# Kernel optimization log

Hardware: AMD Instinct MI355X
Metric: run time of the kernel (lower is better)

The kernel has to match this reference:

```python
import jax, jax.numpy as jnp
import numpy as np

N_NODES = 100_000
N_EDGES = 1_600_000
NUM_GRAPHS = 512
D1, D2, D3, D5, NUM_CLASSES = 3, 50, 15, 10, 6
BN_EPS = 1e-5


def setup_inputs() -> dict:
    key = jax.random.key(0)
    ks = jax.random.split(key, 16)

    def w(k, shape):
        fan_in = shape[0]
        return jax.random.normal(k, shape, jnp.float32) / np.sqrt(fan_in).astype(np.float32)

    return {
        "x": jax.random.normal(ks[0], (N_NODES, D1), jnp.float32),
        "edge_attr": jax.random.normal(ks[1], (N_EDGES, D1), jnp.float32),
        # edge MLP: Lin(9,50) -> ReLU -> Lin(50,15)
        "edge_w1": w(ks[2], (3 * D1, D2)), "edge_b1": jnp.zeros((D2,), jnp.float32),
        "edge_w2": w(ks[3], (D2, D3)), "edge_b2": jnp.zeros((D3,), jnp.float32),
        # node MLP: Lin(18,50) -> ReLU -> Lin(50,15)
        "node_w1": w(ks[4], (D1 + D3, D2)), "node_b1": jnp.zeros((D2,), jnp.float32),
        "node_w2": w(ks[5], (D2, D3)), "node_b2": jnp.zeros((D3,), jnp.float32),
        # readout head
        "fc1_w": w(ks[6], (D3, D5)), "fc1_b": jnp.zeros((D5,), jnp.float32),
        "bn_gamma": jnp.ones((D5,), jnp.float32), "bn_beta": jnp.zeros((D5,), jnp.float32),
        "fc2_w": w(ks[7], (D5, NUM_CLASSES)), "fc2_b": jnp.zeros((NUM_CLASSES,), jnp.float32),
        # graph structure
        "edge_index": jax.random.randint(ks[8], (2, N_EDGES), 0, N_NODES, jnp.int32),
        "batch": jnp.sort(jax.random.randint(ks[9], (N_NODES,), 0, NUM_GRAPHS, jnp.int32)),
    }


def _segment_mean(vals, idx, num_segments):
    s = jax.ops.segment_sum(vals, idx, num_segments=num_segments)
    c = jax.ops.segment_sum(jnp.ones((vals.shape[0], 1), vals.dtype), idx,
                            num_segments=num_segments)
    return s / jnp.maximum(c, 1.0)


def reference(x, edge_attr,
              edge_w1, edge_b1, edge_w2, edge_b2,
              node_w1, node_b1, node_w2, node_b2,
              fc1_w, fc1_b, bn_gamma, bn_beta, fc2_w, fc2_b,
              edge_index, batch):
    row, col = edge_index[0], edge_index[1]
    # edge model: cat([x[row], x[col], edge_attr]) -> MLP  -> [E, D3]
    e_in = jnp.concatenate([x[row], x[col], edge_attr], axis=1)
    edge_attr2 = jax.nn.relu(e_in @ edge_w1 + edge_b1) @ edge_w2 + edge_b2
    # node model: cat([x[col], edge_attr2]) -> MLP -> scatter_mean over row
    n_in = jnp.concatenate([x[col], edge_attr2], axis=1)  # [E, D1+D3]
    msg = jax.nn.relu(n_in @ node_w1 + node_b1) @ node_w2 + node_b2  # [E, D3]
    x2 = _segment_mean(msg, row, x.shape[0])  # [N, D3]
    # global mean pool per graph -> [G, D3]
    u = _segment_mean(x2, batch, NUM_GRAPHS)
    # head: fc1 -> BatchNorm1d (batch stats) -> relu -> fc2 -> log_softmax
    h = u @ fc1_w + fc1_b
    mu = h.mean(axis=0)
    var = h.var(axis=0)  # biased, matches BN training normalization
    h = bn_gamma * (h - mu) * jax.lax.rsqrt(var + BN_EPS) + bn_beta
    h = jax.nn.relu(h)
    logits = h @ fc2_w + fc2_b
    return jax.nn.log_softmax(logits, axis=1)
```

## Files before the change

### kernel.cpp

```cpp
#include <hip/hip_runtime.h>
#include <hip/hip_bf16.h>
#include <math.h>

#define N_NODES    100000
#define N_EDGES    1600000
#define NUM_GRAPHS 512
#define D2 50
#define D3 15
#define D5 10
#define NCLS 6
#define BN_EPS 1e-5f

#define NBLK1 ((N_NODES + 1023) / 1024)

#define W_EW1T 0
#define W_EW2T 2560
#define W_NW1T 3712
#define W_NW2T 6272
#define W_TOTAL 7680

#define EDGE_BLOCKS 2500
#define EDGE_WAVES  (EDGE_BLOCKS * 4)
#define TILES32     (N_EDGES / 32)
#define EDGE_ITERS  (TILES32 / EDGE_WAVES)

typedef __attribute__((ext_vector_type(8))) short short8;
typedef __attribute__((ext_vector_type(4))) float float4_;
union BU { unsigned u[4]; short8 s; };
union FU { unsigned u; float f; };

__device__ __forceinline__ unsigned short f2bf(float f) {
    __hip_bfloat16 h = __float2bfloat16(f);
    union { __hip_bfloat16 h; unsigned short u; } c; c.h = h; return c.u;
}
__device__ __forceinline__ float bf2f(unsigned short u) {
    union { __hip_bfloat16 h; unsigned short u; } c; c.u = u;
    return __bfloat162float(c.h);
}
__device__ __forceinline__ unsigned int pkbf(float a, float b) {
    return (unsigned int)f2bf(a) | ((unsigned int)f2bf(b) << 16);
}
__device__ __forceinline__ unsigned bp(int s4, unsigned v) {
    return (unsigned)__builtin_amdgcn_ds_bpermute(s4, (int)v);
}
__device__ __forceinline__ float lo16(unsigned u) { FU c; c.u = u << 16; return c.f; }
__device__ __forceinline__ float hi16(unsigned u) { FU c; c.u = u & 0xFFFF0000u; return c.f; }

__global__ __launch_bounds__(256) void prep_kernel(
    const float* __restrict__ ew1, const float* __restrict__ eb1,
    const float* __restrict__ ew2, const float* __restrict__ eb2,
    const float* __restrict__ nw1, const float* __restrict__ nb1,
    const float* __restrict__ nw2, const float* __restrict__ nb2,
    unsigned short* __restrict__ wh, unsigned short* __restrict__ wl,
    const float* __restrict__ x, ushort4* __restrict__ x4b,
    const int* __restrict__ edge_index, int* __restrict__ counts)
{
    int gtid = blockIdx.x * 256 + threadIdx.x;
    int gsz = gridDim.x * 256;

    for (int i = gtid; i < W_TOTAL; i += gsz) {
        float v = 0.0f;
        if (i < W_EW2T) {
            int m = i / 40, k = i % 40;
            if (m < 50) {
                if (k < 3)                 v = ew1[k * 50 + m];
                else if (k == 3)           v = eb1[m];
                else if (k >= 4 && k < 7)  v = ew1[(k - 1) * 50 + m];
                else if (k >= 8 && k < 11) v = ew1[(k - 2) * 50 + m];
            }
        } else if (i < W_NW1T) {
            int j = i - W_EW2T; int m = j / 72, k = j % 72;
            if (m < 15) { if (k < 50) v = ew2[k * 15 + m]; else if (k == 50) v = eb2[m]; }
        } else if (i < W_NW2T) {
            int j = i - W_NW1T; int m = j / 40, k = j % 40;
            if (m < 50) {
                if (k < 15)                  v = nw1[(3 + k) * 50 + m];
                else if (k >= 16 && k < 19)  v = nw1[(k - 16) * 50 + m];
                else if (k == 19)            v = nb1[m];
            }
        } else if (i < 7424) {
            int j = i - W_NW2T; int m = j / 72, k = j % 72;
            if (m < 15) { if (k < 50) v = nw2[k * 15 + m]; else if (k == 50) v = nb2[m]; }
        }
        unsigned short h = f2bf(v);
        unsigned short l = f2bf(v - bf2f(h));
        wh[i] = h; wl[i] = l;
    }

    for (int n = gtid; n < N_NODES; n += gsz) {
        ushort4 v;
        v.x = f2bf(x[n * 3 + 0]); v.y = f2bf(x[n * 3 + 1]);
        v.z = f2bf(x[n * 3 + 2]); v.w = 0;
        x4b[n] = v;
    }

    for (int e = gtid; e < N_EDGES; e += gsz)
        atomicAdd(&counts[edge_index[e]], 1);
}

__global__ __launch_bounds__(1024) void scan1_kernel(
    const int* __restrict__ counts, int* __restrict__ scanned, int* __restrict__ bsums)
{
    __shared__ int wsum[16], wofs[16];
    int i = blockIdx.x * 1024 + threadIdx.x;
    int lane = threadIdx.x & 63, wid = threadIdx.x >> 6;
    int v = (i < N_NODES) ? counts[i] : 0;
    int sc = v;
    #pragma unroll
    for (int off = 1; off < 64; off <<= 1) {
        int t = __shfl_up(sc, off);
        if (lane >= off) sc += t;
    }
    if (lane == 63) wsum[wid] = sc;
    __syncthreads();
    if (wid == 0) {
        int s = (lane < 16) ? wsum[lane] : 0;
        #pragma unroll
        for (int off = 1; off < 16; off <<= 1) {
            int t = __shfl_up(s, off);
            if (lane >= off) s += t;
        }
        if (lane < 16) wofs[lane] = s - wsum[lane];
    }
    __syncthreads();
    int incl = sc + wofs[wid];
    if (i < N_NODES) scanned[i] = incl - v;
    if (threadIdx.x == 1023) bsums[blockIdx.x] = incl;
}

__global__ __launch_bounds__(128) void scan2_kernel(
    const int* __restrict__ bsums, int* __restrict__ bofs)
{
    __shared__ int tmp[128];
    int v = (threadIdx.x < NBLK1) ? bsums[threadIdx.x] : 0;
    tmp[threadIdx.x] = v;
    __syncthreads();
    #pragma unroll
    for (int off = 1; off < 128; off <<= 1) {
        int t = (threadIdx.x >= off) ? tmp[threadIdx.x - off] : 0;
        __syncthreads();
        tmp[threadIdx.x] += t;
        __syncthreads();
    }
    if (threadIdx.x < NBLK1) bofs[threadIdx.x] = tmp[threadIdx.x] - v;
}

__global__ __launch_bounds__(256) void scan3_kernel(
    const int* __restrict__ scanned, const int* __restrict__ bofs,
    int* __restrict__ cursor)
{
    int n = blockIdx.x * 256 + threadIdx.x;
    if (n >= N_NODES) return;
    cursor[n] = scanned[n] + bofs[n >> 10];
}

struct EIn { unsigned w0, w1, w2, w3, h0, h1; int pos; };

__device__ __forceinline__ EIn load_in(int ebase, int n, int quad,
    const int* __restrict__ edge_index, const ushort4* __restrict__ x4b,
    const float* __restrict__ edge_attr, int* __restrict__ cursor)
{
    EIn r; r.w0 = r.w1 = r.w2 = r.w3 = 0; r.h0 = r.h1 = 0; r.pos = 0;
    int e = ebase + n;
    if (quad == 0) {
        int row = edge_index[e];
        int col = edge_index[N_EDGES + e];
        ushort4 xr = x4b[row];
        ushort4 xc = x4b[col];
        r.w0 = (unsigned)xr.x | ((unsigned)xr.y << 16);
        r.w1 = (unsigned)xr.z | (0x3F80u << 16);
        r.w2 = (unsigned)xc.x | ((unsigned)xc.y << 16);
        r.w3 = (unsigned)xc.z;
        r.pos = atomicAdd(&cursor[row], 1);
    } else if (quad == 1) {
        r.w0 = pkbf(edge_attr[e * 3 + 0], edge_attr[e * 3 + 1]);
        r.w1 = (unsigned)f2bf(edge_attr[e * 3 + 2]);
    } else if (quad == 2) {
        int col = edge_index[N_EDGES + e];
        ushort4 xc = x4b[col];
        r.h0 = (unsigned)xc.x | ((unsigned)xc.y << 16);
        r.h1 = (unsigned)xc.z | (0x3F80u << 16);
    }
    return r;
}

__device__ __forceinline__ void perm64(const unsigned U[4][2], int s0, int s1, bool hi,
                                       short8& Bc0, short8& Bc1)
{
    BU b0, b1;
    {
        unsigned a0 = bp(s0, U[0][0]), a1 = bp(s0, U[1][0]);
        unsigned a2 = bp(s0, U[0][1]), a3 = bp(s0, U[1][1]);
        unsigned a4 = bp(s1, U[0][0]), a5 = bp(s1, U[1][0]);
        unsigned a6 = bp(s1, U[0][1]), a7 = bp(s1, U[1][1]);
        b0.u[0] = hi ? a1 : a0;
        b0.u[1] = hi ? a3 : a2;
        b0.u[2] = hi ? a5 : a4;
        b0.u[3] = hi ? a7 : a6;
    }
    {
        unsigned a0 = bp(s0, U[2][0]), a1 = bp(s0, U[3][0]);
        unsigned a2 = bp(s0, U[2][1]), a3 = bp(s0, U[3][1]);
        unsigned a4 = bp(s1, U[2][0]), a5 = bp(s1, U[3][0]);
        unsigned a6 = bp(s1, U[2][1]), a7 = bp(s1, U[3][1]);
        b1.u[0] = hi ? a1 : a0;
        b1.u[1] = hi ? a3 : a2;
        b1.u[2] = hi ? a5 : a4;
        b1.u[3] = hi ? a7 : a6;
    }
    Bc0 = b0.s; Bc1 = b1.s;
}

__device__ __forceinline__ short8 perm16(const unsigned U2[2], int s0, int s1,
                                         int quad, unsigned h0, unsigned h1)
{
    BU d;
    d.u[0] = bp(s0, U2[0]);
    d.u[1] = bp(s0, U2[1]);
    d.u[2] = bp(s1, U2[0]);
    d.u[3] = bp(s1, U2[1]);
    if (quad == 2) { d.u[0] = h0; d.u[1] = h1; d.u[2] = 0; d.u[3] = 0; }
    else if (quad == 3) { d.u[0] = 0; d.u[1] = 0; d.u[2] = 0; d.u[3] = 0; }
    return d.s;
}

__global__ __launch_bounds__(256) void edge_mfma_kernel(
    const unsigned short* __restrict__ wh_g, const unsigned short* __restrict__ wl_g,
    const ushort4* __restrict__ x4b, const float* __restrict__ edge_attr,
    const int* __restrict__ edge_index,
    int* __restrict__ cursor, unsigned short* __restrict__ msgb)
{
    int tid = threadIdx.x, wave = tid >> 6, lane = tid & 63;
    int n = lane & 15, quad = lane >> 4;

    short8 A1h[4], A1l[4], A3h[4], A3l[4];
    #pragma unroll
    for (int t4 = 0; t4 < 4; t4++) {
        int o1 = W_EW1T + (t4 * 16 + n) * 40 + quad * 8;
        A1h[t4] = *(const short8*)(wh_g + o1);
        A1l[t4] = *(const short8*)(wl_g + o1);
        int o3 = W_NW1T + (t4 * 16 + n) * 40 + quad * 8;
        A3h[t4] = *(const short8*)(wh_g + o3);
        A3l[t4] = *(const short8*)(wl_g + o3);
    }
    short8 A2h[2], A2l[2], A4h[2], A4l[2];
    #pragma unroll
    for (int kc = 0; kc < 2; kc++) {
        int o2 = W_EW2T + n * 72 + kc * 32 + quad * 8;
        A2h[kc] = *(const short8*)(wh_g + o2);
        A2l[kc] = *(const short8*)(wl_g + o2);
        int o4 = W_NW2T + n * 72 + kc * 32 + quad * 8;
        A4h[kc] = *(const short8*)(wh_g + o4);
        A4l[kc] = *(const short8*)(wl_g + o4);
    }

    int s0 = ((quad & 1) * 32 + n) * 4;
    int s1 = s0 + 64;
    bool hi = (quad & 2) != 0;

    int t = blockIdx.x * 4 + wave;
    EIn cur0 = load_in(t * 32,      n, quad, edge_index, x4b, edge_attr, cursor);
    EIn cur1 = load_in(t * 32 + 16, n, quad, edge_index, x4b, edge_attr, cursor);

    for (int it = 0; it < EDGE_ITERS; it++) {
        int p0 = __shfl(cur0.pos, n);
        int p1 = __shfl(cur1.pos, n);

        int tn = t + EDGE_WAVES;
        EIn nx0, nx1;
        nx0.w0 = nx0.w1 = nx0.w2 = nx0.w3 = nx0.h0 = nx0.h1 = 0; nx0.pos = 0;
        nx1 = nx0;
        if (it + 1 < EDGE_ITERS) {
            nx0 = load_in(tn * 32,      n, quad, edge_index, x4b, edge_attr, cursor);
            nx1 = load_in(tn * 32 + 16, n, quad, edge_index, x4b, edge_attr, cursor);
        }

        BU t0, t1;
        t0.u[0] = cur0.w0; t0.u[1] = cur0.w1; t0.u[2] = cur0.w2; t0.u[3] = cur0.w3;
        t1.u[0] = cur1.w0; t1.u[1] = cur1.w1; t1.u[2] = cur1.w2; t1.u[3] = cur1.w3;
        short8 B1a = t0.s, B1b = t1.s;

        unsigned U1a[4][2], U1b[4][2];
        #pragma unroll
        for (int t4 = 0; t4 < 4; t4++) {
            float4_ za = {0.f, 0.f, 0.f, 0.f}, zb = {0.f, 0.f, 0.f, 0.f};
            za = __builtin_amdgcn_mfma_f32_16x16x32_bf16(A1l[t4], B1a, za, 0, 0, 0);
            zb = __builtin_amdgcn_mfma_f32_16x16x32_bf16(A1l[t4], B1b, zb, 0, 0, 0);
            za = __builtin_amdgcn_mfma_f32_16x16x32_bf16(A1h[t4], B1a, za, 0, 0, 0);
            zb = __builtin_amdgcn_mfma_f32_16x16x32_bf16(A1h[t4], B1b, zb, 0, 0, 0);
            U1a[t4][0] = pkbf(fmaxf(za[0], 0.f), fmaxf(za[1], 0.f));
            U1a[t4][1] = pkbf(fmaxf(za[2], 0.f), fmaxf(za[3], 0.f));
            U1b[t4][0] = pkbf(fmaxf(zb[0], 0.f), fmaxf(zb[1], 0.f));
            U1b[t4][1] = pkbf(fmaxf(zb[2], 0.f), fmaxf(zb[3], 0.f));
        }

        short8 B2a0, B2a1, B2b0, B2b1;
        perm64(U1a, s0, s1, hi, B2a0, B2a1);
        perm64(U1b, s0, s1, hi, B2b0, B2b1);
        if (quad == 2) {
            BU fa, fb; fa.s = B2a1; fb.s = B2b1;
            fa.u[1] = (fa.u[1] & 0xFFFF0000u) | 0x3F80u;
            fb.u[1] = (fb.u[1] & 0xFFFF0000u) | 0x3F80u;
            B2a1 = fa.s; B2b1 = fb.s;
        }

        float4_ a2al = {0.f, 0.f, 0.f, 0.f}, a2ah = {0.f, 0.f, 0.f, 0.f};
        float4_ a2bl = {0.f, 0.f, 0.f, 0.f}, a2bh = {0.f, 0.f, 0.f, 0.f};
        a2al = __builtin_amdgcn_mfma_f32_16x16x32_bf16(A2l[0], B2a0, a2al, 0, 0, 0);
        a2bl = __builtin_amdgcn_mfma_f32_16x16x32_bf16(A2l[0], B2b0, a2bl, 0, 0, 0);
        a2ah = __builtin_amdgcn_mfma_f32_16x16x32_bf16(A2h[0], B2a0, a2ah, 0, 0, 0);
        a2bh = __builtin_amdgcn_mfma_f32_16x16x32_bf16(A2h[0], B2b0, a2bh, 0, 0, 0);
        a2al = __builtin_amdgcn_mfma_f32_16x16x32_bf16(A2l[1], B2a1, a2al, 0, 0, 0);
        a2bl = __builtin_amdgcn_mfma_f32_16x16x32_bf16(A2l[1], B2b1, a2bl, 0, 0, 0);
        a2ah = __builtin_amdgcn_mfma_f32_16x16x32_bf16(A2h[1], B2a1, a2ah, 0, 0, 0);
        a2bh = __builtin_amdgcn_mfma_f32_16x16x32_bf16(A2h[1], B2b1, a2bh, 0, 0, 0);

        unsigned U2a[2] = { pkbf(a2al[0] + a2ah[0], a2al[1] + a2ah[1]),
                            pkbf(a2al[2] + a2ah[2], a2al[3] + a2ah[3]) };
        unsigned U2b[2] = { pkbf(a2bl[0] + a2bh[0], a2bl[1] + a2bh[1]),
                            pkbf(a2bl[2] + a2bh[2], a2bl[3] + a2bh[3]) };

        short8 B3a = perm16(U2a, s0, s1, quad, cur0.h0, cur0.h1);
        short8 B3b = perm16(U2b, s0, s1, quad, cur1.h0, cur1.h1);

        unsigned U3a[4][2], U3b[4][2];
        #pragma unroll
        for (int t4 = 0; t4 < 4; t4++) {
            float4_ za = {0.f, 0.f, 0.f, 0.f}, zb = {0.f, 0.f, 0.f, 0.f};
            za = __builtin_amdgcn_mfma_f32_16x16x32_bf16(A3l[t4], B3a, za, 0, 0, 0);
            zb = __builtin_amdgcn_mfma_f32_16x16x32_bf16(A3l[t4], B3b, zb, 0, 0, 0);
            za = __builtin_amdgcn_mfma_f32_16x16x32_bf16(A3h[t4], B3a, za, 0, 0, 0);
            zb = __builtin_amdgcn_mfma_f32_16x16x32_bf16(A3h[t4], B3b, zb, 0, 0, 0);
            U3a[t4][0] = pkbf(fmaxf(za[0], 0.f), fmaxf(za[1], 0.f));
            U3a[t4][1] = pkbf(fmaxf(za[2], 0.f), fmaxf(za[3], 0.f));
            U3b[t4][0] = pkbf(fmaxf(zb[0], 0.f), fmaxf(zb[1], 0.f));
            U3b[t4][1] = pkbf(fmaxf(zb[2], 0.f), fmaxf(zb[3], 0.f));
        }

        short8 B4a0, B4a1, B4b0, B4b1;
        perm64(U3a, s0, s1, hi, B4a0, B4a1);
        perm64(U3b, s0, s1, hi, B4b0, B4b1);
        if (quad == 2) {
            BU fa, fb; fa.s = B4a1; fb.s = B4b1;
            fa.u[1] = (fa.u[1] & 0xFFFF0000u) | 0x3F80u;
            fb.u[1] = (fb.u[1] & 0xFFFF0000u) | 0x3F80u;
            B4a1 = fa.s; B4b1 = fb.s;
        }

        float4_ mal = {0.f, 0.f, 0.f, 0.f}, mah = {0.f, 0.f, 0.f, 0.f};
        float4_ mbl = {0.f, 0.f, 0.f, 0.f}, mbh = {0.f, 0.f, 0.f, 0.f};
        mal = __builtin_amdgcn_mfma_f32_16x16x32_bf16(A4l[0], B4a0, mal, 0, 0, 0);
        mbl = __builtin_amdgcn_mfma_f32_16x16x32_bf16(A4l[0], B4b0, mbl, 0, 0, 0);
        mah = __builtin_amdgcn_mfma_f32_16x16x32_bf16(A4h[0], B4a0, mah, 0, 0, 0);
        mbh = __builtin_amdgcn_mfma_f32_16x16x32_bf16(A4h[0], B4b0, mbh, 0, 0, 0);
        mal = __builtin_amdgcn_mfma_f32_16x16x32_bf16(A4l[1], B4a1, mal, 0, 0, 0);
        mbl = __builtin_amdgcn_mfma_f32_16x16x32_bf16(A4l[1], B4b1, mbl, 0, 0, 0);
        mah = __builtin_amdgcn_mfma_f32_16x16x32_bf16(A4h[1], B4a1, mah, 0, 0, 0);
        mbh = __builtin_amdgcn_mfma_f32_16x16x32_bf16(A4h[1], B4b1, mbh, 0, 0, 0);

        uint2 pa, pb;
        pa.x = pkbf(mal[0] + mah[0], mal[1] + mah[1]);
        pa.y = pkbf(mal[2] + mah[2], mal[3] + mah[3]);
        pb.x = pkbf(mbl[0] + mbh[0], mbl[1] + mbh[1]);
        pb.y = pkbf(mbl[2] + mbh[2], mbl[3] + mbh[3]);
        *(uint2*)(msgb + (size_t)p0 * 16 + quad * 4) = pa;
        *(uint2*)(msgb + (size_t)p1 * 16 + quad * 4) = pb;

        cur0 = nx0; cur1 = nx1; t = tn;
    }
}

__global__ __launch_bounds__(256) void gather_pool_kernel(
    const unsigned short* __restrict__ msgb, const int* __restrict__ scanned,
    const int* __restrict__ bofs, const int* __restrict__ counts,
    const int* __restrict__ batch, float* __restrict__ gsum)
{
    __shared__ float acc[64 * 16];
    int n0 = blockIdx.x * 256;
    int n = n0 + threadIdx.x;

    float v[16];
    #pragma unroll
    for (int k = 0; k < 16; k++) v[k] = 0.0f;
    if (n < N_NODES) {
        int start = scanned[n] + bofs[n >> 10];
        int deg = counts[n];
        for (int j = 0; j < deg; j++) {
            const uint4* mp = (const uint4*)(msgb + (size_t)(start + j) * 16);
            uint4 qa = mp[0], qb = mp[1];
            v[0]  += lo16(qa.x); v[1]  += hi16(qa.x);
            v[2]  += lo16(qa.y); v[3]  += hi16(qa.y);
            v[4]  += lo16(qa.z); v[5]  += hi16(qa.z);
            v[6]  += lo16(qa.w); v[7]  += hi16(qa.w);
            v[8]  += lo16(qb.x); v[9]  += hi16(qb.x);
            v[10] += lo16(qb.y); v[11] += hi16(qb.y);
            v[12] += lo16(qb.z); v[13] += hi16(qb.z);
            v[14] += lo16(qb.w);
        }
        float inv = 1.0f / fmaxf((float)deg, 1.0f);
        #pragma unroll
        for (int k = 0; k < 15; k++) v[k] *= inv;
        v[15] = 1.0f;
    }

    int gmin = batch[n0];
    int gmax = batch[min(n0 + 255, N_NODES - 1)];
    int range = gmax - gmin + 1;
    if (range <= 64) {
        for (int t = threadIdx.x; t < range * 16; t += 256) acc[t] = 0.0f;
        __syncthreads();
        if (n < N_NODES) {
            int g = batch[n] - gmin;
            float* dst = &acc[g * 16];
            #pragma unroll
            for (int k = 0; k < 16; k++) atomicAdd(&dst[k], v[k]);
        }
        __syncthreads();
        for (int t = threadIdx.x; t < range * 16; t += 256) {
            float w = acc[t];
            if (w != 0.0f) atomicAdd(&gsum[(size_t)gmin * 16 + t], w);
        }
    } else {
        if (n < N_NODES) {
            int g = batch[n];
            float* dst = gsum + (size_t)g * 16;
            #pragma unroll
            for (int k = 0; k < 16; k++) atomicAdd(&dst[k], v[k]);
        }
    }
}

__global__ __launch_bounds__(512) void head_kernel(
    const float* __restrict__ gsum,
    const float* __restrict__ fc1w, const float* __restrict__ fc1b,
    const float* __restrict__ gamma, const float* __restrict__ beta,
    const float* __restrict__ fc2w, const float* __restrict__ fc2b,
    float* __restrict__ out)
{
    __shared__ float ssum[D5], ssq[D5], smu[D5], sistd[D5];
    int g = threadIdx.x;
    if (g < D5) { ssum[g] = 0.0f; ssq[g] = 0.0f; }
    __syncthreads();

    const float* src = gsum + (size_t)g * 16;
    float inv = 1.0f / fmaxf(src[15], 1.0f);
    float u[D3];
    #pragma unroll
    for (int k = 0; k < D3; k++) u[k] = src[k] * inv;

    float h[D5];
    #pragma unroll
    for (int c = 0; c < D5; c++) h[c] = fc1b[c];
    #pragma unroll
    for (int k = 0; k < D3; k++) {
        float v = u[k];
        #pragma unroll
        for (int c = 0; c < D5; c++) h[c] = fmaf(v, fc1w[k * D5 + c], h[c]);
    }

    int lane = threadIdx.x & 63;
    #pragma unroll
    for (int c = 0; c < D5; c++) {
        float v = h[c];
        float v2 = v * v;
        #pragma unroll
        for (int off = 32; off >= 1; off >>= 1) {
            v  += __shfl_xor(v,  off);
            v2 += __shfl_xor(v2, off);
        }
        if (lane == 0) { atomicAdd(&ssum[c], v); atomicAdd(&ssq[c], v2); }
    }
    __syncthreads();
    if (g < D5) {
        float mu = ssum[g] * (1.0f / NUM_GRAPHS);
        float var = ssq[g] * (1.0f / NUM_GRAPHS) - mu * mu;
        smu[g] = mu;
        sistd[g] = rsqrtf(var + BN_EPS);
    }
    __syncthreads();

    float hn[D5];
    #pragma unroll
    for (int c = 0; c < D5; c++) {
        float v = gamma[c] * (h[c] - smu[c]) * sistd[c] + beta[c];
        hn[c] = fmaxf(v, 0.0f);
    }

    float lg[NCLS];
    #pragma unroll
    for (int j = 0; j < NCLS; j++) lg[j] = fc2b[j];
    #pragma unroll
    for (int c = 0; c < D5; c++) {
        float v = hn[c];
        #pragma unroll
        for (int j = 0; j < NCLS; j++) lg[j] = fmaf(v, fc2w[c * NCLS + j], lg[j]);
    }

    float m = lg[0];
    #pragma unroll
    for (int j = 1; j < NCLS; j++) m = fmaxf(m, lg[j]);
    float se = 0.0f;
    #pragma unroll
    for (int j = 0; j < NCLS; j++) se += expf(lg[j] - m);
    float lse = logf(se);
    #pragma unroll
    for (int j = 0; j < NCLS; j++) out[g * NCLS + j] = lg[j] - m - lse;
}

extern "C" void kernel_launch(void* const* d_in, const int* in_sizes, int n_in,
                              void* d_out, int out_size, void* d_ws, size_t ws_size,
                              hipStream_t stream) {
    const float* x         = (const float*)d_in[0];
    const float* edge_attr = (const float*)d_in[1];
    const float* ew1  = (const float*)d_in[2];
    const float* eb1  = (const float*)d_in[3];
    const float* ew2  = (const float*)d_in[4];
    const float* eb2  = (const float*)d_in[5];
    const float* nw1  = (const float*)d_in[6];
    const float* nb1  = (const float*)d_in[7];
    const float* nw2  = (const float*)d_in[8];
    const float* nb2  = (const float*)d_in[9];
    const float* fc1w = (const float*)d_in[10];
    const float* fc1b = (const float*)d_in[11];
    const float* gamma= (const float*)d_in[12];
    const float* beta = (const float*)d_in[13];
    const float* fc2w = (const float*)d_in[14];
    const float* fc2b = (const float*)d_in[15];
    const int* edge_index = (const int*)d_in[16];
    const int* batch      = (const int*)d_in[17];

    char* p = (char*)d_ws;
    unsigned short* msgb = (unsigned short*)p; p += (size_t)N_EDGES * 16 * sizeof(unsigned short);
    int* counts  = (int*)p;            p += (size_t)N_NODES * sizeof(int);
    int* scanned = (int*)p;            p += (size_t)N_NODES * sizeof(int);
    int* cursor  = (int*)p;            p += (size_t)N_NODES * sizeof(int);
    int* bsums   = (int*)p;            p += 128 * sizeof(int);
    int* bofs    = (int*)p;            p += 128 * sizeof(int);
    ushort4* x4b = (ushort4*)p;        p += (size_t)N_NODES * sizeof(ushort4);
    float* gsum  = (float*)p;          p += (size_t)NUM_GRAPHS * 16 * sizeof(float);
    unsigned short* wh = (unsigned short*)p; p += W_TOTAL * sizeof(unsigned short);
    unsigned short* wl = (unsigned short*)p; p += W_TOTAL * sizeof(unsigned short);

    hipMemsetAsync(counts, 0, (size_t)N_NODES * sizeof(int), stream);
    hipMemsetAsync(gsum, 0, (size_t)NUM_GRAPHS * 16 * sizeof(float), stream);

    int egrid = (N_EDGES + 255) / 256;
    int ngrid = (N_NODES + 255) / 256;

    prep_kernel<<<egrid, 256, 0, stream>>>(
        ew1, eb1, ew2, eb2, nw1, nb1, nw2, nb2, wh, wl,
        x, x4b, edge_index, counts);
    scan1_kernel<<<NBLK1, 1024, 0, stream>>>(counts, scanned, bsums);
    scan2_kernel<<<1, 128, 0, stream>>>(bsums, bofs);
    scan3_kernel<<<ngrid, 256, 0, stream>>>(scanned, bofs, cursor);
    edge_mfma_kernel<<<EDGE_BLOCKS, 256, 0, stream>>>(
        wh, wl, x4b, edge_attr, edge_index, cursor, msgb);
    gather_pool_kernel<<<ngrid, 256, 0, stream>>>(
        msgb, scanned, bofs, counts, batch, gsum);
    head_kernel<<<1, 512, 0, stream>>>(
        gsum, fc1w, fc1b, gamma, beta, fc2w, fc2b, (float*)d_out);
}
```

Before: 373.2 us.

## Drop hi/lo split-bf16 weights and fuse three-pass scan into one atomic scan

Weights for the edge and node MLPs were stored as a high and a low bf16 pair, which doubled the MFMA count per layer. Only the single bf16 part is kept now, so each layer does half the MFMAs and loads half the weight registers. Separately, the three scan kernels become one: each block takes its global base offset with an atomicAdd on a counter, which removes two launches and the bofs indirection. The risks are reduced accuracy from single-bf16 weights, and CSR segment order that now depends on block scheduling, though the segments stay valid and do not overlap.

After: 328.4 us. -12.0%, faster.

```diff
diff --git a/kernel.cpp b/kernel.cpp
--- a/kernel.cpp
+++ b/kernel.cpp
@@ -33,10 +33,6 @@
     __hip_bfloat16 h = __float2bfloat16(f);
     union { __hip_bfloat16 h; unsigned short u; } c; c.h = h; return c.u;
 }
-__device__ __forceinline__ float bf2f(unsigned short u) {
-    union { __hip_bfloat16 h; unsigned short u; } c; c.u = u;
-    return __bfloat162float(c.h);
-}
 __device__ __forceinline__ unsigned int pkbf(float a, float b) {
     return (unsigned int)f2bf(a) | ((unsigned int)f2bf(b) << 16);
 }
@@ -51,7 +47,7 @@
     const float* __restrict__ ew2, const float* __restrict__ eb2,
     const float* __restrict__ nw1, const float* __restrict__ nb1,
     const float* __restrict__ nw2, const float* __restrict__ nb2,
-    unsigned short* __restrict__ wh, unsigned short* __restrict__ wl,
+    unsigned short* __restrict__ wh,
     const float* __restrict__ x, ushort4* __restrict__ x4b,
     const int* __restrict__ edge_index, int* __restrict__ counts)
 {
@@ -82,9 +78,7 @@
             int j = i - W_NW2T; int m = j / 72, k = j % 72;
             if (m < 15) { if (k < 50) v = nw2[k * 15 + m]; else if (k == 50) v = nb2[m]; }
         }
-        unsigned short h = f2bf(v);
-        unsigned short l = f2bf(v - bf2f(h));
-        wh[i] = h; wl[i] = l;
+        wh[i] = f2bf(v);
     }
 
     for (int n = gtid; n < N_NODES; n += gsz) {
@@ -98,10 +92,12 @@
         atomicAdd(&counts[edge_index[e]], 1);
 }
 
-__global__ __launch_bounds__(1024) void scan1_kernel(
-    const int* __restrict__ counts, int* __restrict__ scanned, int* __restrict__ bsums)
+__global__ __launch_bounds__(1024) void scan_kernel(
+    const int* __restrict__ counts, int* __restrict__ scanned,
+    int* __restrict__ cursor, int* __restrict__ gctr)
 {
     __shared__ int wsum[16], wofs[16];
+    __shared__ int base;
     int i = blockIdx.x * 1024 + threadIdx.x;
     int lane = threadIdx.x & 63, wid = threadIdx.x >> 6;
     int v = (i < N_NODES) ? counts[i] : 0;
@@ -124,34 +120,10 @@
     }
     __syncthreads();
     int incl = sc + wofs[wid];
-    if (i < N_NODES) scanned[i] = incl - v;
-    if (threadIdx.x == 1023) bsums[blockIdx.x] = incl;
-}
-
-__global__ __launch_bounds__(128) void scan2_kernel(
-    const int* __restrict__ bsums, int* __restrict__ bofs)
-{
-    __shared__ int tmp[128];
-    int v = (threadIdx.x < NBLK1) ? bsums[threadIdx.x] : 0;
-    tmp[threadIdx.x] = v;
+    if (threadIdx.x == 1023) base = atomicAdd(gctr, incl);
     __syncthreads();
-    #pragma unroll
-    for (int off = 1; off < 128; off <<= 1) {
-        int t = (threadIdx.x >= off) ? tmp[threadIdx.x - off] : 0;
-        __syncthreads();
-        tmp[threadIdx.x] += t;
-        __syncthreads();
-    }
-    if (threadIdx.x < NBLK1) bofs[threadIdx.x] = tmp[threadIdx.x] - v;
-}
-
-__global__ __launch_bounds__(256) void scan3_kernel(
-    const int* __restrict__ scanned, const int* __restrict__ bofs,
-    int* __restrict__ cursor)
-{
-    int n = blockIdx.x * 256 + threadIdx.x;
-    if (n >= N_NODES) return;
-    cursor[n] = scanned[n] + bofs[n >> 10];
+    int start = base + incl - v;
+    if (i < N_NODES) { scanned[i] = start; cursor[i] = start; }
 }
 
 struct EIn { unsigned w0, w1, w2, w3, h0, h1; int pos; };
@@ -225,7 +197,7 @@
 }
 
 __global__ __launch_bounds__(256) void edge_mfma_kernel(
-    const unsigned short* __restrict__ wh_g, const unsigned short* __restrict__ wl_g,
+    const unsigned short* __restrict__ wh_g,
     const ushort4* __restrict__ x4b, const float* __restrict__ edge_attr,
     const int* __restrict__ edge_index,
     int* __restrict__ cursor, unsigned short* __restrict__ msgb)
@@ -233,25 +205,17 @@
     int tid = threadIdx.x, wave = tid >> 6, lane = tid & 63;
     int n = lane & 15, quad = lane >> 4;
 
-    short8 A1h[4], A1l[4], A3h[4], A3l[4];
+    short8 A1[4], A3[4];
     #pragma unroll
     for (int t4 = 0; t4 < 4; t4++) {
-        int o1 = W_EW1T + (t4 * 16 + n) * 40 + quad * 8;
-        A1h[t4] = *(const short8*)(wh_g + o1);
-        A1l[t4] = *(const short8*)(wl_g + o1);
-        int o3 = W_NW1T + (t4 * 16 + n) * 40 + quad * 8;
-        A3h[t4] = *(const short8*)(wh_g + o3);
-        A3l[t4] = *(const short8*)(wl_g + o3);
-    }
-    short8 A2h[2], A2l[2], A4h[2], A4l[2];
+        A1[t4] = *(const short8*)(wh_g + W_EW1T + (t4 * 16 + n) * 40 + quad * 8);
+        A3[t4] = *(const short8*)(wh_g + W_NW1T + (t4 * 16 + n) * 40 + quad * 8);
+    }
+    short8 A2[2], A4[2];
     #pragma unroll
     for (int kc = 0; kc < 2; kc++) {
-        int o2 = W_EW2T + n * 72 + kc * 32 + quad * 8;
-        A2h[kc] = *(const short8*)(wh_g + o2);
-        A2l[kc] = *(const short8*)(wl_g + o2);
-        int o4 = W_NW2T + n * 72 + kc * 32 + quad * 8;
-        A4h[kc] = *(const short8*)(wh_g + o4);
-        A4l[kc] = *(const short8*)(wl_g + o4);
+        A2[kc] = *(const short8*)(wh_g + W_EW2T + n * 72 + kc * 32 + quad * 8);
+        A4[kc] = *(const short8*)(wh_g + W_NW2T + n * 72 + kc * 32 + quad * 8);
     }
 
     int s0 = ((quad & 1) * 32 + n) * 4;
@@ -284,10 +248,8 @@
         #pragma unroll
         for (int t4 = 0; t4 < 4; t4++) {
             float4_ za = {0.f, 0.f, 0.f, 0.f}, zb = {0.f, 0.f, 0.f, 0.f};
-            za = __builtin_amdgcn_mfma_f32_16x16x32_bf16(A1l[t4], B1a, za, 0, 0, 0);
-            zb = __builtin_amdgcn_mfma_f32_16x16x32_bf16(A1l[t4], B1b, zb, 0, 0, 0);
-            za = __builtin_amdgcn_mfma_f32_16x16x32_bf16(A1h[t4], B1a, za, 0, 0, 0);
-            zb = __builtin_amdgcn_mfma_f32_16x16x32_bf16(A1h[t4], B1b, zb, 0, 0, 0);
+            za = __builtin_amdgcn_mfma_f32_16x16x32_bf16(A1[t4], B1a, za, 0, 0, 0);
+            zb = __builtin_amdgcn_mfma_f32_16x16x32_bf16(A1[t4], B1b, zb, 0, 0, 0);
             U1a[t4][0] = pkbf(fmaxf(za[0], 0.f), fmaxf(za[1], 0.f));
             U1a[t4][1] = pkbf(fmaxf(za[2], 0.f), fmaxf(za[3], 0.f));
             U1b[t4][0] = pkbf(fmaxf(zb[0], 0.f), fmaxf(zb[1], 0.f));
@@ -304,21 +266,14 @@
             B2a1 = fa.s; B2b1 = fb.s;
         }
 
-        float4_ a2al = {0.f, 0.f, 0.f, 0.f}, a2ah = {0.f, 0.f, 0.f, 0.f};
-        float4_ a2bl = {0.f, 0.f, 0.f, 0.f}, a2bh = {0.f, 0.f, 0.f, 0.f};
-        a2al = __builtin_amdgcn_mfma_f32_16x16x32_bf16(A2l[0], B2a0, a2al, 0, 0, 0);
-        a2bl = __builtin_amdgcn_mfma_f32_16x16x32_bf16(A2l[0], B2b0, a2bl, 0, 0, 0);
-        a2ah = __builtin_amdgcn_mfma_f32_16x16x32_bf16(A2h[0], B2a0, a2ah, 0, 0, 0);
-        a2bh = __builtin_amdgcn_mfma_f32_16x16x32_bf16(A2h[0], B2b0, a2bh, 0, 0, 0);
-        a2al = __builtin_amdgcn_mfma_f32_16x16x32_bf16(A2l[1], B2a1, a2al, 0, 0, 0);
-        a2bl = __builtin_amdgcn_mfma_f32_16x16x32_bf16(A2l[1], B2b1, a2bl, 0, 0, 0);
-        a2ah = __builtin_amdgcn_mfma_f32_16x16x32_bf16(A2h[1], B2a1, a2ah, 0, 0, 0);
-        a2bh = __builtin_amdgcn_mfma_f32_16x16x32_bf16(A2h[1], B2b1, a2bh, 0, 0, 0);
-
-        unsigned U2a[2] = { pkbf(a2al[0] + a2ah[0], a2al[1] + a2ah[1]),
-                            pkbf(a2al[2] + a2ah[2], a2al[3] + a2ah[3]) };
-        unsigned U2b[2] = { pkbf(a2bl[0] + a2bh[0], a2bl[1] + a2bh[1]),
-                            pkbf(a2bl[2] + a2bh[2], a2bl[3] + a2bh[3]) };
+        float4_ a2a = {0.f, 0.f, 0.f, 0.f}, a2b = {0.f, 0.f, 0.f, 0.f};
+        a2a = __builtin_amdgcn_mfma_f32_16x16x32_bf16(A2[0], B2a0, a2a, 0, 0, 0);
+        a2b = __builtin_amdgcn_mfma_f32_16x16x32_bf16(A2[0], B2b0, a2b, 0, 0, 0);
+        a2a = __builtin_amdgcn_mfma_f32_16x16x32_bf16(A2[1], B2a1, a2a, 0, 0, 0);
+        a2b = __builtin_amdgcn_mfma_f32_16x16x32_bf16(A2[1], B2b1, a2b, 0, 0, 0);
+
+        unsigned U2a[2] = { pkbf(a2a[0], a2a[1]), pkbf(a2a[2], a2a[3]) };
+        unsigned U2b[2] = { pkbf(a2b[0], a2b[1]), pkbf(a2b[2], a2b[3]) };
 
         short8 B3a = perm16(U2a, s0, s1, quad, cur0.h0, cur0.h1);
         short8 B3b = perm16(U2b, s0, s1, quad, cur1.h0, cur1.h1);
@@ -327,10 +282,8 @@
         #pragma unroll
         for (int t4 = 0; t4 < 4; t4++) {
             float4_ za = {0.f, 0.f, 0.f, 0.f}, zb = {0.f, 0.f, 0.f, 0.f};
-            za = __builtin_amdgcn_mfma_f32_16x16x32_bf16(A3l[t4], B3a, za, 0, 0, 0);
-            zb = __builtin_amdgcn_mfma_f32_16x16x32_bf16(A3l[t4], B3b, zb, 0, 0, 0);
-            za = __builtin_amdgcn_mfma_f32_16x16x32_bf16(A3h[t4], B3a, za, 0, 0, 0);
-            zb = __builtin_amdgcn_mfma_f32_16x16x32_bf16(A3h[t4], B3b, zb, 0, 0, 0);
+            za = __builtin_amdgcn_mfma_f32_16x16x32_bf16(A3[t4], B3a, za, 0, 0, 0);
+            zb = __builtin_amdgcn_mfma_f32_16x16x32_bf16(A3[t4], B3b, zb, 0, 0, 0);
             U3a[t4][0] = pkbf(fmaxf(za[0], 0.f), fmaxf(za[1], 0.f));
             U3a[t4][1] = pkbf(fmaxf(za[2], 0.f), fmaxf(za[3], 0.f));
             U3b[t4][0] = pkbf(fmaxf(zb[0], 0.f), fmaxf(zb[1], 0.f));
@@ -347,22 +300,15 @@
             B4a1 = fa.s; B4b1 = fb.s;
         }
 
-        float4_ mal = {0.f, 0.f, 0.f, 0.f}, mah = {0.f, 0.f, 0.f, 0.f};
-        float4_ mbl = {0.f, 0.f, 0.f, 0.f}, mbh = {0.f, 0.f, 0.f, 0.f};
-        mal = __builtin_amdgcn_mfma_f32_16x16x32_bf16(A4l[0], B4a0, mal, 0, 0, 0);
-        mbl = __builtin_amdgcn_mfma_f32_16x16x32_bf16(A4l[0], B4b0, mbl, 0, 0, 0);
-        mah = __builtin_amdgcn_mfma_f32_16x16x32_bf16(A4h[0], B4a0, mah, 0, 0, 0);
-        mbh = __builtin_amdgcn_mfma_f32_16x16x32_bf16(A4h[0], B4b0, mbh, 0, 0, 0);
-        mal = __builtin_amdgcn_mfma_f32_16x16x32_bf16(A4l[1], B4a1, mal, 0, 0, 0);
-        mbl = __builtin_amdgcn_mfma_f32_16x16x32_bf16(A4l[1], B4b1, mbl, 0, 0, 0);
-        mah = __builtin_amdgcn_mfma_f32_16x16x32_bf16(A4h[1], B4a1, mah, 0, 0, 0);
-        mbh = __builtin_amdgcn_mfma_f32_16x16x32_bf16(A4h[1], B4b1, mbh, 0, 0, 0);
+        float4_ ma = {0.f, 0.f, 0.f, 0.f}, mb = {0.f, 0.f, 0.f, 0.f};
+        ma = __builtin_amdgcn_mfma_f32_16x16x32_bf16(A4[0], B4a0, ma, 0, 0, 0);
+        mb = __builtin_amdgcn_mfma_f32_16x16x32_bf16(A4[0], B4b0, mb, 0, 0, 0);
+        ma = __builtin_amdgcn_mfma_f32_16x16x32_bf16(A4[1], B4a1, ma, 0, 0, 0);
+        mb = __builtin_amdgcn_mfma_f32_16x16x32_bf16(A4[1], B4b1, mb, 0, 0, 0);
 
         uint2 pa, pb;
-        pa.x = pkbf(mal[0] + mah[0], mal[1] + mah[1]);
-        pa.y = pkbf(mal[2] + mah[2], mal[3] + mah[3]);
-        pb.x = pkbf(mbl[0] + mbh[0], mbl[1] + mbh[1]);
-        pb.y = pkbf(mbl[2] + mbh[2], mbl[3] + mbh[3]);
+        pa.x = pkbf(ma[0], ma[1]); pa.y = pkbf(ma[2], ma[3]);
+        pb.x = pkbf(mb[0], mb[1]); pb.y = pkbf(mb[2], mb[3]);
         *(uint2*)(msgb + (size_t)p0 * 16 + quad * 4) = pa;
         *(uint2*)(msgb + (size_t)p1 * 16 + quad * 4) = pb;
 
@@ -372,8 +318,8 @@
 
 __global__ __launch_bounds__(256) void gather_pool_kernel(
     const unsigned short* __restrict__ msgb, const int* __restrict__ scanned,
-    const int* __restrict__ bofs, const int* __restrict__ counts,
-    const int* __restrict__ batch, float* __restrict__ gsum)
+    const int* __restrict__ counts, const int* __restrict__ batch,
+    float* __restrict__ gsum)
 {
     __shared__ float acc[64 * 16];
     int n0 = blockIdx.x * 256;
@@ -383,7 +329,7 @@
     #pragma unroll
     for (int k = 0; k < 16; k++) v[k] = 0.0f;
     if (n < N_NODES) {
-        int start = scanned[n] + bofs[n >> 10];
+        int start = scanned[n];
         int deg = counts[n];
         for (int j = 0; j < deg; j++) {
             const uint4* mp = (const uint4*)(msgb + (size_t)(start + j) * 16);
@@ -532,31 +478,27 @@
     char* p = (char*)d_ws;
     unsigned short* msgb = (unsigned short*)p; p += (size_t)N_EDGES * 16 * sizeof(unsigned short);
     int* counts  = (int*)p;            p += (size_t)N_NODES * sizeof(int);
+    int* gctr    = (int*)p;            p += sizeof(int);
     int* scanned = (int*)p;            p += (size_t)N_NODES * sizeof(int);
     int* cursor  = (int*)p;            p += (size_t)N_NODES * sizeof(int);
-    int* bsums   = (int*)p;            p += 128 * sizeof(int);
-    int* bofs    = (int*)p;            p += 128 * sizeof(int);
     ushort4* x4b = (ushort4*)p;        p += (size_t)N_NODES * sizeof(ushort4);
     float* gsum  = (float*)p;          p += (size_t)NUM_GRAPHS * 16 * sizeof(float);
     unsigned short* wh = (unsigned short*)p; p += W_TOTAL * sizeof(unsigned short);
-    unsigned short* wl = (unsigned short*)p; p += W_TOTAL * sizeof(unsigned short);
-
-    hipMemsetAsync(counts, 0, (size_t)N_NODES * sizeof(int), stream);
+
+    hipMemsetAsync(counts, 0, (size_t)(N_NODES + 1) * sizeof(int), stream);
     hipMemsetAsync(gsum, 0, (size_t)NUM_GRAPHS * 16 * sizeof(float), stream);
 
     int egrid = (N_EDGES + 255) / 256;
     int ngrid = (N_NODES + 255) / 256;
 
     prep_kernel<<<egrid, 256, 0, stream>>>(
-        ew1, eb1, ew2, eb2, nw1, nb1, nw2, nb2, wh, wl,
+        ew1, eb1, ew2, eb2, nw1, nb1, nw2, nb2, wh,
         x, x4b, edge_index, counts);
-    scan1_kernel<<<NBLK1, 1024, 0, stream>>>(counts, scanned, bsums);
-    scan2_kernel<<<1, 128, 0, stream>>>(bsums, bofs);
-    scan3_kernel<<<ngrid, 256, 0, stream>>>(scanned, bofs, cursor);
+    scan_kernel<<<NBLK1, 1024, 0, stream>>>(counts, scanned, cursor, gctr);
     edge_mfma_kernel<<<EDGE_BLOCKS, 256, 0, stream>>>(
-        wh, wl, x4b, edge_attr, edge_index, cursor, msgb);
+        wh, x4b, edge_attr, edge_index, cursor, msgb);
     gather_pool_kernel<<<ngrid, 256, 0, stream>>>(
-        msgb, scanned, bofs, counts, batch, gsum);
+        msgb, scanned, counts, batch, gsum);
     head_kernel<<<1, 512, 0, stream>>>(
         gsum, fc1w, fc1b, gamma, beta, fc2w, fc2b, (float*)d_out);
 }
```
